# Kernel tuning notes

Hardware: AMD Instinct MI355X
Metric: run time of the kernel (lower is better)

## Reference

```python
import jax, jax.numpy as jnp
import numpy as np

K = 2  # top-k experts per token


def setup_inputs() -> dict:
    key = jax.random.key(0)
    kx, kw = jax.random.split(key)
    N, D, E = 16384, 4096, 64
    x = jax.random.normal(kx, (N, D), dtype=jnp.float32)
    # nn.Linear(input_dim, num_experts, bias=False) weight: [num_experts, input_dim]
    W = jax.random.normal(kw, (E, D), dtype=jnp.float32) * (1.0 / np.sqrt(D))
    return {"x": x, "W": W}


def reference(x, W):
    # logits = x @ W^T : [N, E]
    logits = jnp.einsum('nd,ed->ne', x, W)
    top_k_logits, top_k_indices = jax.lax.top_k(logits, K)  # [N, K]
    top_k_weights = jax.nn.softmax(top_k_logits, axis=-1)   # softmax over the k selected
    N = logits.shape[0]
    rows = jnp.arange(N)[:, None]  # [N, 1] broadcast against [N, K]
    full_weights = jnp.zeros_like(logits).at[rows, top_k_indices].set(top_k_weights)
    return full_weights, top_k_indices
```

## Files before the change

### kernel.cpp

```cpp
#include <hip/hip_runtime.h>
#include <math.h>

#define N_TOK 16384
#define DDIM  4096
#define NEXP  64
#define TM    32
#define WINF  256
#define NSTEP (DDIM / WINF)
#define LSTR  68
#define TAU   1e-3f

typedef __attribute__((ext_vector_type(8))) short bf16x8;
typedef __attribute__((ext_vector_type(4))) float f32x4;

__device__ __forceinline__ void split8(f32x4 v0, f32x4 v1, bf16x8& hi, bf16x8& lo) {
    float f[8];
    *(f32x4*)&f[0] = v0;  *(f32x4*)&f[4] = v1;
    #pragma unroll
    for (int i = 0; i < 8; ++i) {
        unsigned u  = __float_as_uint(f[i]);
        unsigned uh = u & 0xFFFF0000u;
        float    rf = f[i] - __uint_as_float(uh);
        hi[i] = (short)(u >> 16);
        lo[i] = (short)(__float_as_uint(rf) >> 16);
    }
}

__global__ __launch_bounds__(256) void pack_w_kernel(
    const float* __restrict__ W, short* __restrict__ Wp)
{
    const int c    = blockIdx.x;
    const int tid  = threadIdx.x;
    const int t    = tid >> 6;
    const int lane = tid & 63;
    const int r16  = lane & 15;
    const int koct = lane >> 4;
    const float* src = W + (size_t)(t * 16 + r16) * DDIM + c * 32 + koct * 8;
    f32x4 b0 = *(const f32x4*)src;
    f32x4 b1 = *(const f32x4*)(src + 4);
    bf16x8 hi, lo;
    split8(b0, b1, hi, lo);
    short* d = Wp + ((size_t)(c * 4 + t) * 2) * 512 + lane * 8;
    *(bf16x8*)d         = hi;
    *(bf16x8*)(d + 512) = lo;
}

__global__ __launch_bounds__(512, 4) void topk_gate_kernel(
    const float* __restrict__ x, const short* __restrict__ Wp,
    const float* __restrict__ W, float* __restrict__ out)
{
    __shared__ __align__(16) char sraw[73728];
    __shared__ int    top_i[TM * 2];
    __shared__ float  top_w[TM * 2];
    __shared__ int    nflag;
    __shared__ int    flist[TM];
    __shared__ double lgd[NEXP];
    __shared__ int    rbi[2];
    __shared__ float  rbw[2];

    const int tid  = threadIdx.x;
    const int lane = tid & 63;
    const int w    = tid >> 6;
    const int block_tok = blockIdx.x * TM;
    const int phase = (blockIdx.x >> 3) & 15;
    const int r16  = lane & 15;
    const int koct = lane >> 4;
    const int m    = (r16 & 7) << 4;
    const int o0   = w * 128 + koct * 32;

    const char* xrow = (const char*)x
                     + (size_t)(block_tok + w * 4) * (DDIM * 4) + lane * 16;
    const int sw0 = (lane * 16) ^ ((((w * 4) + 0) & 7) << 4);
    const int sw1 = (lane * 16) ^ ((((w * 4) + 1) & 7) << 4);
    const int sw2 = (lane * 16) ^ ((((w * 4) + 2) & 7) << 4);
    const int sw3 = (lane * 16) ^ ((((w * 4) + 3) & 7) << 4);
    char* const wbase = sraw + (w * 4) * 1024;

    f32x4 rA0, rA1, rA2, rA3, rB0, rB1, rB2, rB3;

#define LOADR(a0, a1, a2, a3, S) do {                                        \
    const char* _s = xrow + (size_t)(S) * 1024;                              \
    a0 = *(const f32x4*)(_s);                                                \
    a1 = *(const f32x4*)(_s + 16384);                                        \
    a2 = *(const f32x4*)(_s + 32768);                                        \
    a3 = *(const f32x4*)(_s + 49152);                                        \
} while (0)

#define WRITER(a0, a1, a2, a3, B) do {                                       \
    char* _d = wbase + (B) * 32768;                                          \
    *(f32x4*)(_d +        sw0) = a0;                                         \
    *(f32x4*)(_d + 1024 + sw1) = a1;                                         \
    *(f32x4*)(_d + 2048 + sw2) = a2;                                         \
    *(f32x4*)(_d + 3072 + sw3) = a3;                                         \
} while (0)

    f32x4 acc[2][4];
    #pragma unroll
    for (int tt = 0; tt < 2; ++tt)
        #pragma unroll
        for (int t = 0; t < 4; ++t) acc[tt][t] = (f32x4){0.f, 0.f, 0.f, 0.f};

#define COMPUTE(B, S) do {                                                   \
    const char* _buf = sraw + (B) * 32768;                                   \
    const int _cg = (S) * 8 + w;                         \
    bf16x8 ah[2], al[2];                                                     \
    _Pragma("unroll")                                                        \
    for (int tt = 0; tt < 2; ++tt) {                                         \
        const char* xb = _buf + ((tt * 16 + r16) << 10);                     \
        f32x4 a0 = *(const f32x4*)(xb + (o0 ^ m));                           \
        f32x4 a1 = *(const f32x4*)(xb + ((o0 + 16) ^ m));                    \
        split8(a0, a1, ah[tt], al[tt]);                                      \
    }                                                                        \
    _Pragma("unroll")                                                        \
    for (int t = 0; t < 4; ++t) {                                            \
        const short* wb = Wp + ((size_t)(_cg * 4 + t) * 2) * 512 + lane * 8; \
        bf16x8 bh = *(const bf16x8*)wb;                                      \
        bf16x8 bl = *(const bf16x8*)(wb + 512);                              \
        _Pragma("unroll")                                                    \
        for (int tt = 0; tt < 2; ++tt) {                                     \
            acc[tt][t] = __builtin_amdgcn_mfma_f32_16x16x32_bf16(ah[tt], bh, acc[tt][t], 0, 0, 0); \
            acc[tt][t] = __builtin_amdgcn_mfma_f32_16x16x32_bf16(ah[tt], bl, acc[tt][t], 0, 0, 0); \
            acc[tt][t] = __builtin_amdgcn_mfma_f32_16x16x32_bf16(al[tt], bh, acc[tt][t], 0, 0, 0); \
        }                                                                    \
    }                                                                        \
} while (0)

    LOADR(rA0, rA1, rA2, rA3, (phase + 0) & 15);
    LOADR(rB0, rB1, rB2, rB3, (phase + 1) & 15);
    #pragma unroll 1
    for (int si = 0; si < NSTEP; si += 2) {
        WRITER(rA0, rA1, rA2, rA3, 0);
        __syncthreads();
        if (si + 2 < NSTEP) LOADR(rA0, rA1, rA2, rA3, (phase + si + 2) & 15);
        COMPUTE(0, (phase + si) & 15);
        __syncthreads();
        WRITER(rB0, rB1, rB2, rB3, 1);
        __syncthreads();
        if (si + 3 < NSTEP) LOADR(rB0, rB1, rB2, rB3, (phase + si + 3) & 15);
        COMPUTE(1, (phase + si + 1) & 15);
        __syncthreads();
    }
#undef LOADR
#undef WRITER
#undef COMPUTE

    float* Lg = (float*)sraw;
    #pragma unroll
    for (int tt = 0; tt < 2; ++tt)
        #pragma unroll
        for (int t = 0; t < 4; ++t)
            #pragma unroll
            for (int r = 0; r < 4; ++r)
                Lg[(w * TM + tt * 16 + koct * 4 + r) * LSTR + t * 16 + r16] = acc[tt][t][r];
    if (tid == 0) nflag = 0;
    __syncthreads();

    {
        const int tok = tid >> 4;
        const int e4  = (tid & 15) * 4;
        float4 s0 = *(float4*)&Lg[(0 * TM + tok) * LSTR + e4];
        #pragma unroll
        for (int qq = 1; qq < 8; ++qq) {
            float4 v = *(float4*)&Lg[(qq * TM + tok) * LSTR + e4];
            s0.x += v.x; s0.y += v.y; s0.z += v.z; s0.w += v.w;
        }
        *(float4*)&Lg[tok * LSTR + e4] = s0;
    }
    __syncthreads();

    if (tid < TM) {
        float m1 = -INFINITY, m2 = -INFINITY, m3 = -INFINITY;
        int i1 = 0, i2 = 0;
        for (int e = 0; e < NEXP; ++e) {
            float v = Lg[tid * LSTR + e];
            if (v > m1)      { m3 = m2; m2 = m1; i2 = i1; m1 = v; i1 = e; }
            else if (v > m2) { m3 = m2; m2 = v; i2 = e; }
            else if (v > m3) { m3 = v; }
        }
        float d  = expf(m2 - m1);
        float rn = 1.0f / (1.0f + d);
        top_i[tid * 2 + 0] = i1;  top_i[tid * 2 + 1] = i2;
        top_w[tid * 2 + 0] = rn;  top_w[tid * 2 + 1] = d * rn;
        float2* oi = (float2*)(out + (size_t)N_TOK * NEXP);
        oi[block_tok + tid] = make_float2((float)i1, (float)i2);
        if ((m1 - m2 < TAU) || (m2 - m3 < TAU)) {
            int pp = atomicAdd(&nflag, 1);
            flist[pp] = tid;
        }
    }
    __syncthreads();

    {
        float4* ow = (float4*)(out + (size_t)block_tok * NEXP);
        const int tok = tid >> 4;
        const int e4  = (tid & 15) * 4;
        int a1 = top_i[tok * 2], a2 = top_i[tok * 2 + 1];
        float v1 = top_w[tok * 2], v2 = top_w[tok * 2 + 1];
        float4 v; float* vp = (float*)&v;
        #pragma unroll
        for (int q = 0; q < 4; ++q) {
            int e = e4 + q;
            vp[q] = (e == a1) ? v1 : ((e == a2) ? v2 : 0.0f);
        }
        ow[tid] = v;
    }
    __syncthreads();

    double* red = (double*)(sraw + 69632);
    const int fn = nflag;
    for (int f = 0; f < fn; ++f) {
        const int tok = block_tok + flist[f];
        {
            const int e = tid & 63, q = tid >> 6;
            const float* wr = W + (size_t)e * DDIM + q * (DDIM / 8);
            const float* xr = x + (size_t)tok * DDIM + q * (DDIM / 8);
            double pp = 0.0;
            for (int k = 0; k < DDIM / 8; k += 4) {
                float4 wv = *(const float4*)(wr + k);
                float4 xv = *(const float4*)(xr + k);
                pp += (double)xv.x * (double)wv.x;
                pp += (double)xv.y * (double)wv.y;
                pp += (double)xv.z * (double)wv.z;
                pp += (double)xv.w * (double)wv.w;
            }
            red[tid] = pp;
        }
        __syncthreads();
        if (tid < 64) {
            double s = 0.0;
            #pragma unroll
            for (int j = 0; j < 8; ++j) s += red[tid + 64 * j];
            lgd[tid] = s;
        }
        __syncthreads();

        if (tid == 0) {
            double m1 = -INFINITY, m2 = -INFINITY;
            int i1 = 0, i2 = 0;
            for (int ee = 0; ee < NEXP; ++ee) {
                double v = lgd[ee];
                if (v > m1)      { m2 = m1; i2 = i1; m1 = v; i1 = ee; }
                else if (v > m2) { m2 = v; i2 = ee; }
            }
            double d  = exp(m2 - m1);
            double rn = 1.0 / (1.0 + d);
            rbi[0] = i1; rbi[1] = i2;
            rbw[0] = (float)rn; rbw[1] = (float)(d * rn);
            float2* oi = (float2*)(out + (size_t)N_TOK * NEXP);
            oi[tok] = make_float2((float)i1, (float)i2);
        }
        __syncthreads();

        if (tid < 16) {
            float4 v = make_float4(0.f, 0.f, 0.f, 0.f);
            float* vp = (float*)&v;
            #pragma unroll
            for (int qq = 0; qq < 4; ++qq) {
                int ee = tid * 4 + qq;
                if (ee == rbi[0]) vp[qq] = rbw[0];
                else if (ee == rbi[1]) vp[qq] = rbw[1];
            }
            ((float4*)(out + (size_t)tok * NEXP))[tid] = v;
        }
        __syncthreads();
    }
}

extern "C" void kernel_launch(void* const* d_in, const int* in_sizes, int n_in,
                              void* d_out, int out_size, void* d_ws, size_t ws_size,
                              hipStream_t stream) {
    const float* x = (const float*)d_in[0];
    const float* W = (const float*)d_in[1];
    float* out = (float*)d_out;
    short* Wp  = (short*)d_ws;
    (void)in_sizes; (void)n_in; (void)ws_size; (void)out_size;

    hipLaunchKernelGGL(pack_w_kernel, dim3(DDIM / 32), dim3(256), 0, stream, W, Wp);
    hipLaunchKernelGGL(topk_gate_kernel, dim3(N_TOK / TM), dim3(512), 0, stream,
                       x, Wp, W, out);
}
```

Measured before the change: 502.6 us.

## Double token tile to 64 with 16 waves splitting experts across wave halves

Each block now handles 64 tokens with 1024 threads. Waves are split into 8 K-column groups times 2 expert halves, so each wave does 4 token sub-tiles × 2 expert tiles, halving per-token loads of the packed W fragments. The x staging buffer doubles to 64KB per stage, and register prefetch drops from two stages to one. This reduces redundant W traffic but gives up some latency hiding on the x loads, and the much larger LDS footprint limits the CU to one block.

New measurement: 514.1 us. 2.3% more time.

```diff
diff --git a/kernel.cpp b/kernel.cpp
--- a/kernel.cpp
+++ b/kernel.cpp
@@ -4,7 +4,8 @@
 #define N_TOK 16384
 #define DDIM  4096
 #define NEXP  64
-#define TM    32
+#define TM    64
+#define NW    16
 #define WINF  256
 #define NSTEP (DDIM / WINF)
 #define LSTR  68
@@ -45,11 +46,11 @@
     *(bf16x8*)(d + 512) = lo;
 }
 
-__global__ __launch_bounds__(512, 4) void topk_gate_kernel(
+__global__ __launch_bounds__(1024, 4) void topk_gate_kernel(
     const float* __restrict__ x, const short* __restrict__ Wp,
     const float* __restrict__ W, float* __restrict__ out)
 {
-    __shared__ __align__(16) char sraw[73728];
+    __shared__ __align__(16) char sraw[147456];
     __shared__ int    top_i[TM * 2];
     __shared__ float  top_w[TM * 2];
     __shared__ int    nflag;
@@ -61,12 +62,14 @@
     const int tid  = threadIdx.x;
     const int lane = tid & 63;
     const int w    = tid >> 6;
+    const int cj   = w & 7;
+    const int th   = w >> 3;
     const int block_tok = blockIdx.x * TM;
     const int phase = (blockIdx.x >> 3) & 15;
     const int r16  = lane & 15;
     const int koct = lane >> 4;
     const int m    = (r16 & 7) << 4;
-    const int o0   = w * 128 + koct * 32;
+    const int o0   = cj * 128 + koct * 32;
 
     const char* xrow = (const char*)x
                      + (size_t)(block_tok + w * 4) * (DDIM * 4) + lane * 16;
@@ -76,48 +79,49 @@
     const int sw3 = (lane * 16) ^ ((((w * 4) + 3) & 7) << 4);
     char* const wbase = sraw + (w * 4) * 1024;
 
-    f32x4 rA0, rA1, rA2, rA3, rB0, rB1, rB2, rB3;
-
-#define LOADR(a0, a1, a2, a3, S) do {                                        \
+    f32x4 r0, r1, r2, r3;
+
+#define LOADR(S) do {                                                        \
     const char* _s = xrow + (size_t)(S) * 1024;                              \
-    a0 = *(const f32x4*)(_s);                                                \
-    a1 = *(const f32x4*)(_s + 16384);                                        \
-    a2 = *(const f32x4*)(_s + 32768);                                        \
-    a3 = *(const f32x4*)(_s + 49152);                                        \
+    r0 = *(const f32x4*)(_s);                                                \
+    r1 = *(const f32x4*)(_s + 16384);                                        \
+    r2 = *(const f32x4*)(_s + 32768);                                        \
+    r3 = *(const f32x4*)(_s + 49152);                                        \
 } while (0)
 
-#define WRITER(a0, a1, a2, a3, B) do {                                       \
-    char* _d = wbase + (B) * 32768;                                          \
-    *(f32x4*)(_d +        sw0) = a0;                                         \
-    *(f32x4*)(_d + 1024 + sw1) = a1;                                         \
-    *(f32x4*)(_d + 2048 + sw2) = a2;                                         \
-    *(f32x4*)(_d + 3072 + sw3) = a3;                                         \
+#define WRITER(B) do {                                                       \
+    char* _d = wbase + (B) * 65536;                                          \
+    *(f32x4*)(_d +        sw0) = r0;                                         \
+    *(f32x4*)(_d + 1024 + sw1) = r1;                                         \
+    *(f32x4*)(_d + 2048 + sw2) = r2;                                         \
+    *(f32x4*)(_d + 3072 + sw3) = r3;                                         \
 } while (0)
 
-    f32x4 acc[2][4];
+    f32x4 acc[4][2];
     #pragma unroll
-    for (int tt = 0; tt < 2; ++tt)
-        #pragma unroll
-        for (int t = 0; t < 4; ++t) acc[tt][t] = (f32x4){0.f, 0.f, 0.f, 0.f};
+    for (int tt = 0; tt < 4; ++tt)
+        #pragma unroll
+        for (int t = 0; t < 2; ++t) acc[tt][t] = (f32x4){0.f, 0.f, 0.f, 0.f};
 
 #define COMPUTE(B, S) do {                                                   \
-    const char* _buf = sraw + (B) * 32768;                                   \
-    const int _cg = (S) * 8 + w;                         \
-    bf16x8 ah[2], al[2];                                                     \
+    const char* _buf = sraw + (B) * 65536;                                   \
+    const int _cg = (S) * 8 + cj;                        \
+    bf16x8 ah[4], al[4];                                                     \
     _Pragma("unroll")                                                        \
-    for (int tt = 0; tt < 2; ++tt) {                                         \
+    for (int tt = 0; tt < 4; ++tt) {                                         \
         const char* xb = _buf + ((tt * 16 + r16) << 10);                     \
         f32x4 a0 = *(const f32x4*)(xb + (o0 ^ m));                           \
         f32x4 a1 = *(const f32x4*)(xb + ((o0 + 16) ^ m));                    \
         split8(a0, a1, ah[tt], al[tt]);                                      \
     }                                                                        \
     _Pragma("unroll")                                                        \
-    for (int t = 0; t < 4; ++t) {                                            \
-        const short* wb = Wp + ((size_t)(_cg * 4 + t) * 2) * 512 + lane * 8; \
+    for (int t = 0; t < 2; ++t) {                                            \
+        const int T = th * 2 + t;                                            \
+        const short* wb = Wp + ((size_t)(_cg * 4 + T) * 2) * 512 + lane * 8; \
         bf16x8 bh = *(const bf16x8*)wb;                                      \
         bf16x8 bl = *(const bf16x8*)(wb + 512);                              \
         _Pragma("unroll")                                                    \
-        for (int tt = 0; tt < 2; ++tt) {                                     \
+        for (int tt = 0; tt < 4; ++tt) {                                     \
             acc[tt][t] = __builtin_amdgcn_mfma_f32_16x16x32_bf16(ah[tt], bh, acc[tt][t], 0, 0, 0); \
             acc[tt][t] = __builtin_amdgcn_mfma_f32_16x16x32_bf16(ah[tt], bl, acc[tt][t], 0, 0, 0); \
             acc[tt][t] = __builtin_amdgcn_mfma_f32_16x16x32_bf16(al[tt], bh, acc[tt][t], 0, 0, 0); \
@@ -125,19 +129,13 @@
     }                                                                        \
 } while (0)
 
-    LOADR(rA0, rA1, rA2, rA3, (phase + 0) & 15);
-    LOADR(rB0, rB1, rB2, rB3, (phase + 1) & 15);
+    LOADR((phase + 0) & 15);
     #pragma unroll 1
-    for (int si = 0; si < NSTEP; si += 2) {
-        WRITER(rA0, rA1, rA2, rA3, 0);
-        __syncthreads();
-        if (si + 2 < NSTEP) LOADR(rA0, rA1, rA2, rA3, (phase + si + 2) & 15);
-        COMPUTE(0, (phase + si) & 15);
-        __syncthreads();
-        WRITER(rB0, rB1, rB2, rB3, 1);
-        __syncthreads();
-        if (si + 3 < NSTEP) LOADR(rB0, rB1, rB2, rB3, (phase + si + 3) & 15);
-        COMPUTE(1, (phase + si + 1) & 15);
+    for (int si = 0; si < NSTEP; ++si) {
+        WRITER(si & 1);
+        __syncthreads();
+        if (si + 1 < NSTEP) LOADR((phase + si + 1) & 15);
+        COMPUTE(si & 1, (phase + si) & 15);
         __syncthreads();
     }
 #undef LOADR
@@ -146,12 +144,13 @@
 
     float* Lg = (float*)sraw;
     #pragma unroll
-    for (int tt = 0; tt < 2; ++tt)
-        #pragma unroll
-        for (int t = 0; t < 4; ++t)
+    for (int tt = 0; tt < 4; ++tt)
+        #pragma unroll
+        for (int t = 0; t < 2; ++t)
             #pragma unroll
             for (int r = 0; r < 4; ++r)
-                Lg[(w * TM + tt * 16 + koct * 4 + r) * LSTR + t * 16 + r16] = acc[tt][t][r];
+                Lg[(cj * TM + tt * 16 + koct * 4 + r) * LSTR
+                   + th * 32 + t * 16 + r16] = acc[tt][t][r];
     if (tid == 0) nflag = 0;
     __syncthreads();
 
@@ -206,16 +205,16 @@
     }
     __syncthreads();
 
-    double* red = (double*)(sraw + 69632);
+    double* red = (double*)(sraw + 139264);
     const int fn = nflag;
     for (int f = 0; f < fn; ++f) {
         const int tok = block_tok + flist[f];
         {
             const int e = tid & 63, q = tid >> 6;
-            const float* wr = W + (size_t)e * DDIM + q * (DDIM / 8);
-            const float* xr = x + (size_t)tok * DDIM + q * (DDIM / 8);
+            const float* wr = W + (size_t)e * DDIM + q * (DDIM / 16);
+            const float* xr = x + (size_t)tok * DDIM + q * (DDIM / 16);
             double pp = 0.0;
-            for (int k = 0; k < DDIM / 8; k += 4) {
+            for (int k = 0; k < DDIM / 16; k += 4) {
                 float4 wv = *(const float4*)(wr + k);
                 float4 xv = *(const float4*)(xr + k);
                 pp += (double)xv.x * (double)wv.x;
@@ -229,7 +228,7 @@
         if (tid < 64) {
             double s = 0.0;
             #pragma unroll
-            for (int j = 0; j < 8; ++j) s += red[tid + 64 * j];
+            for (int j = 0; j < 16; ++j) s += red[tid + 64 * j];
             lgd[tid] = s;
         }
         __syncthreads();
@@ -276,6 +275,6 @@
     (void)in_sizes; (void)n_in; (void)ws_size; (void)out_size;
 
     hipLaunchKernelGGL(pack_w_kernel, dim3(DDIM / 32), dim3(256), 0, stream, W, Wp);
-    hipLaunchKernelGGL(topk_gate_kernel, dim3(N_TOK / TM), dim3(512), 0, stream,
+    hipLaunchKernelGGL(topk_gate_kernel, dim3(N_TOK / TM), dim3(1024), 0, stream,
                        x, Wp, W, out);
 }
```

## Deepen x prefetch to four register sets with four-slot LDS ring

Applied to the files above, without the earlier changes.

Replaces the two-buffer LDS double-buffering with a four-slot ring buffer and four register sets of prefetched x data, loading four steps ahead. Each step needs only one barrier instead of two, using raw s_barrier with sched_barriers to pin instruction order, and the loop is fully unrolled. Shared memory grows to 128 KB and launch bounds drop to 2 blocks per CU. This trades occupancy and register pressure for more in-flight global loads and fewer synchronizations.

Measured after the change: 475.4 us. -5.4%, faster.

```diff
diff --git a/kernel.cpp b/kernel.cpp
--- a/kernel.cpp
+++ b/kernel.cpp
@@ -45,11 +45,11 @@
     *(bf16x8*)(d + 512) = lo;
 }
 
-__global__ __launch_bounds__(512, 4) void topk_gate_kernel(
+__global__ __launch_bounds__(512, 2) void topk_gate_kernel(
     const float* __restrict__ x, const short* __restrict__ Wp,
     const float* __restrict__ W, float* __restrict__ out)
 {
-    __shared__ __align__(16) char sraw[73728];
+    __shared__ __align__(16) char sraw[131072];
     __shared__ int    top_i[TM * 2];
     __shared__ float  top_w[TM * 2];
     __shared__ int    nflag;
@@ -74,9 +74,9 @@
     const int sw1 = (lane * 16) ^ ((((w * 4) + 1) & 7) << 4);
     const int sw2 = (lane * 16) ^ ((((w * 4) + 2) & 7) << 4);
     const int sw3 = (lane * 16) ^ ((((w * 4) + 3) & 7) << 4);
-    char* const wbase = sraw + (w * 4) * 1024;
-
-    f32x4 rA0, rA1, rA2, rA3, rB0, rB1, rB2, rB3;
+
+    f32x4 pA0, pA1, pA2, pA3, pB0, pB1, pB2, pB3;
+    f32x4 pC0, pC1, pC2, pC3, pD0, pD1, pD2, pD3;
 
 #define LOADR(a0, a1, a2, a3, S) do {                                        \
     const char* _s = xrow + (size_t)(S) * 1024;                              \
@@ -86,8 +86,8 @@
     a3 = *(const f32x4*)(_s + 49152);                                        \
 } while (0)
 
-#define WRITER(a0, a1, a2, a3, B) do {                                       \
-    char* _d = wbase + (B) * 32768;                                          \
+#define WRITER(a0, a1, a2, a3, SLOT) do {                                    \
+    char* _d = sraw + (SLOT) * 32768 + (w * 4) * 1024;                       \
     *(f32x4*)(_d +        sw0) = a0;                                         \
     *(f32x4*)(_d + 1024 + sw1) = a1;                                         \
     *(f32x4*)(_d + 2048 + sw2) = a2;                                         \
@@ -100,9 +100,9 @@
         #pragma unroll
         for (int t = 0; t < 4; ++t) acc[tt][t] = (f32x4){0.f, 0.f, 0.f, 0.f};
 
-#define COMPUTE(B, S) do {                                                   \
-    const char* _buf = sraw + (B) * 32768;                                   \
-    const int _cg = (S) * 8 + w;                         \
+#define COMPUTE(SLOT, SWIN) do {                                             \
+    const char* _buf = sraw + (SLOT) * 32768;                                \
+    const int _cg = (SWIN) * 8 + w;                      \
     bf16x8 ah[2], al[2];                                                     \
     _Pragma("unroll")                                                        \
     for (int tt = 0; tt < 2; ++tt) {                                         \
@@ -125,24 +125,32 @@
     }                                                                        \
 } while (0)
 
-    LOADR(rA0, rA1, rA2, rA3, (phase + 0) & 15);
-    LOADR(rB0, rB1, rB2, rB3, (phase + 1) & 15);
-    #pragma unroll 1
-    for (int si = 0; si < NSTEP; si += 2) {
-        WRITER(rA0, rA1, rA2, rA3, 0);
-        __syncthreads();
-        if (si + 2 < NSTEP) LOADR(rA0, rA1, rA2, rA3, (phase + si + 2) & 15);
-        COMPUTE(0, (phase + si) & 15);
-        __syncthreads();
-        WRITER(rB0, rB1, rB2, rB3, 1);
-        __syncthreads();
-        if (si + 3 < NSTEP) LOADR(rB0, rB1, rB2, rB3, (phase + si + 3) & 15);
-        COMPUTE(1, (phase + si + 1) & 15);
-        __syncthreads();
+#define STEP(S, a0, a1, a2, a3) do {                                         \
+    WRITER(a0, a1, a2, a3, (S) & 3);   \
+    asm volatile("s_waitcnt lgkmcnt(0)" ::: "memory");                       \
+    __builtin_amdgcn_sched_barrier(0);                                       \
+    __builtin_amdgcn_s_barrier();                                            \
+    __builtin_amdgcn_sched_barrier(0);                                       \
+    if ((S) + 4 < NSTEP) LOADR(a0, a1, a2, a3, (phase + (S) + 4) & 15);      \
+    __builtin_amdgcn_sched_barrier(0);                                       \
+    COMPUTE((S) & 3, (phase + (S)) & 15);                                    \
+} while (0)
+
+    LOADR(pA0, pA1, pA2, pA3, (phase + 0) & 15);
+    LOADR(pB0, pB1, pB2, pB3, (phase + 1) & 15);
+    LOADR(pC0, pC1, pC2, pC3, (phase + 2) & 15);
+    LOADR(pD0, pD1, pD2, pD3, (phase + 3) & 15);
+    #pragma unroll
+    for (int sb = 0; sb < NSTEP; sb += 4) {
+        STEP(sb + 0, pA0, pA1, pA2, pA3);
+        STEP(sb + 1, pB0, pB1, pB2, pB3);
+        STEP(sb + 2, pC0, pC1, pC2, pC3);
+        STEP(sb + 3, pD0, pD1, pD2, pD3);
     }
 #undef LOADR
 #undef WRITER
 #undef COMPUTE
+#undef STEP
 
     float* Lg = (float*)sraw;
     #pragma unroll
```
